# Kernel tuning notes

Measured on AMD Instinct MI355X. Metric: run time of the kernel, lower is better.

Reference implementation:

```python
import jax, jax.numpy as jnp
from jax import lax
import numpy as np

B, C, L, H, W = 2, 64, 16, 64, 64
K = 7
NG = 4  # GroupNorm groups (SpatialGroupNorm(4, channels))


def setup_inputs() -> dict:
    key = jax.random.key(0)
    ks = jax.random.split(key, 16)
    s = lambda i, shape, sc: jax.random.normal(ks[i], shape, jnp.float32) * sc
    return {
        "x": s(0, (B, C, L, H, W), 1.0),
        "dt": jax.random.uniform(ks[1], (B, L), jnp.float32, 0.1, 1.0),
        "W_sp": s(2, (C, C, K, K), 0.02),      # spatial 7x7 conv (OIHW)
        "W_dc": s(3, (C, C), 0.1),             # 1x1x1 depth conv
        "b_dc": jnp.zeros((C,), jnp.float32),
        "gn_g": jnp.ones((C,), jnp.float32),
        "gn_b": jnp.zeros((C,), jnp.float32),
        "W_in": s(4, (2 * C, C), 0.1),         # pw_conv_in 1x1 -> 2C (gated)
        "b_in": jnp.zeros((2 * C,), jnp.float32),
        "W_out": s(5, (C, C), 0.1),            # pw_conv_out 1x1
        "b_out": jnp.zeros((C,), jnp.float32),
        "nu_log": s(6, (C,), 0.5),             # LRU log decay rate
        "theta_log": s(7, (C,), 0.5),          # LRU log frequency
        "c_re": s(8, (C,), 0.5),               # LRU output mix (real)
        "c_im": s(9, (C,), 0.5),               # LRU output mix (imag)
        "d_skip": s(10, (C,), 0.5),            # LRU feedthrough
    }


def reference(x, dt, W_sp, W_dc, b_dc, gn_g, gn_b, W_in, b_in, W_out, b_out,
              nu_log, theta_log, c_re, c_im, d_skip):
    Bb, Cc, Ll, Hh, Ww = x.shape
    pad = W_sp.shape[-1] // 2
    # --- GatedConvBlock: FactorizedPeriodicConv3d (per-frame 2D conv) ---
    xf = x.transpose(0, 2, 1, 3, 4).reshape(Bb * Ll, Cc, Hh, Ww)  # [B*L,C,H,W]
    xp = jnp.pad(xf, ((0, 0), (0, 0), (0, 0), (pad, pad)), mode='wrap')    # circular W
    xp = jnp.pad(xp, ((0, 0), (0, 0), (pad, pad), (0, 0)), mode='edge')    # replicate H
    y = lax.conv_general_dilated(xp, W_sp, (1, 1), 'VALID',
                                 dimension_numbers=('NCHW', 'OIHW', 'NCHW'))
    y = jnp.einsum('nchw,oc->nohw', y, W_dc) + b_dc[None, :, None, None]   # depth 1x1x1
    # --- SpatialGroupNorm (per frame, 4 groups) ---
    g = y.reshape(Bb * Ll, NG, Cc // NG, Hh, Ww)
    mu = g.mean(axis=(2, 3, 4), keepdims=True)
    var = g.var(axis=(2, 3, 4), keepdims=True)
    y = ((g - mu) * lax.rsqrt(var + 1e-5)).reshape(Bb * Ll, Cc, Hh, Ww)
    y = y * gn_g[None, :, None, None] + gn_b[None, :, None, None]
    # --- gated pointwise convs + residual ---
    h = jnp.einsum('nchw,oc->nohw', y, W_in) + b_in[None, :, None, None]
    x1, x2 = jnp.split(h, 2, axis=1)
    z = x1 * jax.nn.sigmoid(x2)
    z = jnp.einsum('nchw,oc->nohw', z, W_out) + b_out[None, :, None, None]
    u = xf + z                                     # residual, [B*L,C,H,W]
    u = u.reshape(Bb, Ll, Cc, Hh, Ww).transpose(1, 0, 2, 3, 4)  # [L,B,C,H,W]
    # --- LRU: dt-dependent complex diagonal recurrence over L ---
    decay = jnp.exp(-jnp.exp(nu_log)[None, None, :] * dt[:, :, None])   # [B,L,C]
    phase = jnp.exp(theta_log)[None, None, :] * dt[:, :, None]          # [B,L,C]
    lam_re = (decay * jnp.cos(phase)).transpose(1, 0, 2)[..., None, None]  # [L,B,C,1,1]
    lam_im = (decay * jnp.sin(phase)).transpose(1, 0, 2)[..., None, None]
    gamma = jnp.sqrt(jnp.maximum(1.0 - decay ** 2, 1e-6)).transpose(1, 0, 2)[..., None, None]
    cr = c_re[None, :, None, None]
    ci = c_im[None, :, None, None]
    ds = d_skip[None, :, None, None]

    def step(carry, inputs):
        h_re, h_im = carry
        ut, lr, li, gm = inputs
        nr = lr * h_re - li * h_im + gm * ut
        ni = li * h_re + lr * h_im
        yt = cr * nr + ci * ni + ds * ut
        return (nr, ni), yt

    init = (jnp.zeros((Bb, Cc, Hh, Ww), x.dtype), jnp.zeros((Bb, Cc, Hh, Ww), x.dtype))
    _, ys = lax.scan(step, init, (u, lam_re, lam_im, gamma))   # ys: [L,B,C,H,W]
    return ys.transpose(1, 2, 0, 3, 4)                         # [B,C,L,H,W]
```

## Files before the change

### kernel.cpp

```cpp
#include <hip/hip_runtime.h>
#include <hip/hip_bf16.h>

typedef short bf16x8 __attribute__((ext_vector_type(8)));
typedef float f32x16 __attribute__((ext_vector_type(16)));

#define B_ 2
#define C_ 64
#define L_ 16
#define N_ 32
#define HW_ 4096

#define BY_WPH  0u
#define BY_WP1  401408u
#define BY_WP2  434176u
#define BY_OFF1 450560u
#define BY_LR   451072u
#define BY_LI   459264u
#define BY_GM   467456u
#define BY_PART 475648u
#define BY_XHI  524288u
#define BY_U    524288u

__device__ __forceinline__ unsigned short f2bf(float v) {
    unsigned int u = __float_as_uint(v);
    unsigned int r = u + 0x7FFFu + ((u >> 16) & 1u);
    return (unsigned short)(r >> 16);
}
__device__ __forceinline__ float bf2f(unsigned short s) {
    return __uint_as_float(((unsigned int)s) << 16);
}

__global__ void k_pack(const float* __restrict__ W_sp, const float* __restrict__ W_dc,
                       unsigned short* __restrict__ WpH) {
    int idx = blockIdx.x * 256 + threadIdx.x;
    if (idx >= 49 * 512) return;
    int lane = idx & 63;
    int ks   = (idx >> 6) & 3;
    int nf   = (idx >> 8) & 1;
    int tap  = idx >> 9;
    int oc   = nf * 32 + (lane & 31);
    int icb  = ks * 16 + (lane >> 5) * 8;
    unsigned short h8[8];
    #pragma unroll
    for (int e = 0; e < 8; ++e) {
        int ic = icb + e;
        float s = 0.f;
        for (int c = 0; c < 64; ++c)
            s += W_dc[oc * 64 + c] * W_sp[(c * 64 + ic) * 49 + tap];
        h8[e] = f2bf(s);
    }
    #pragma unroll
    for (int e = 0; e < 8; ++e) WpH[idx * 8 + e] = h8[e];
}

__global__ void k_prep(const float* __restrict__ W_in, const float* __restrict__ b_in,
                       const float* __restrict__ W_out,
                       const float* __restrict__ gn_g, const float* __restrict__ gn_b,
                       unsigned short* __restrict__ WP1, unsigned short* __restrict__ WP2,
                       float* __restrict__ OFF1) {
    int idx = blockIdx.x * 256 + threadIdx.x;
    if (idx < 2048) {
        int lane = idx & 63, ks = (idx >> 6) & 3, nf = (idx >> 8) & 3, hl = idx >> 10;
        int o = nf * 32 + (lane & 31), cb = ks * 16 + (lane >> 5) * 8;
        #pragma unroll
        for (int e = 0; e < 8; ++e) {
            float v = W_in[o * 64 + cb + e] * gn_g[cb + e];
            unsigned short h = f2bf(v);
            WP1[idx * 8 + e] = hl ? f2bf(v - bf2f(h)) : h;
        }
    } else if (idx < 3072) {
        int i2 = idx - 2048;
        int lane = i2 & 63, ks = (i2 >> 6) & 3, nf = (i2 >> 8) & 1, hl = i2 >> 9;
        int j = nf * 32 + (lane & 31), ob = ks * 16 + (lane >> 5) * 8;
        #pragma unroll
        for (int e = 0; e < 8; ++e) {
            float v = W_out[j * 64 + ob + e];
            unsigned short h = f2bf(v);
            WP2[i2 * 8 + e] = hl ? f2bf(v - bf2f(h)) : h;
        }
    } else if (idx < 3200) {
        int o = idx - 3072;
        float s = b_in[o];
        for (int c = 0; c < 64; ++c) s += W_in[o * 64 + c] * gn_b[c];
        OFF1[o] = s;
    }
}

__global__ void k_lam(const float* __restrict__ dt, const float* __restrict__ nu_log,
                      const float* __restrict__ theta_log,
                      float* __restrict__ lr_t, float* __restrict__ li_t, float* __restrict__ gm_t) {
    int idx = blockIdx.x * 256 + threadIdx.x;
    if (idx >= N_ * C_) return;
    int c = idx & 63, n = idx >> 6;
    float dtv = dt[n];
    float decay = expf(-expf(nu_log[c]) * dtv);
    float phase = expf(theta_log[c]) * dtv;
    lr_t[idx] = decay * cosf(phase);
    li_t[idx] = decay * sinf(phase);
    gm_t[idx] = sqrtf(fmaxf(1.f - decay * decay, 1e-6f));
}

__global__ __launch_bounds__(256) void k_tr(const float* __restrict__ x,
                                            unsigned short* __restrict__ xhi) {
    __shared__ float t[64][129];
    int blk = blockIdx.x;
    int n = blk >> 5, seg = blk & 31;
    int p0 = seg * 128;
    int b = n >> 4, l = n & 15;
    int tid = threadIdx.x;
    for (int i = 0; i < 32; ++i) {
        int idx = i * 256 + tid;
        int ic = idx >> 7, p = idx & 127;
        t[ic][p] = x[(((size_t)(b * 64 + ic) * 16 + l)) * 4096 + p0 + p];
    }
    __syncthreads();
    for (int it = 0; it < 4; ++it) {
        int chunk = it * 256 + tid;
        int p = chunk >> 3, c0 = (chunk & 7) * 8;
        unsigned short h8[8];
        #pragma unroll
        for (int e = 0; e < 8; ++e) h8[e] = f2bf(t[c0 + e][p]);
        size_t off = ((size_t)(n * 4096 + p0 + p)) * 64 + c0;
        *(uint4*)&xhi[off] = *(uint4*)h8;
    }
}

__global__ __launch_bounds__(256, 2) void k_conv(
    const unsigned short* __restrict__ xhi,
    const unsigned short* __restrict__ WpH,
    const float* __restrict__ b_dc, float* __restrict__ y,
    float* __restrict__ part) {
    __shared__ uint4 halo[3904];
    __shared__ float ps[4][8], pq[4][8];
    int tid = threadIdx.x;
    int tile = blockIdx.x;
    int th = tile >> 2, tw = tile & 3;
    int n = blockIdx.y;
    int lane = tid & 63, wid = tid >> 6;
    int dh = (lane >> 4) & 1, dw = lane & 15, kslot = lane >> 5;

    for (int u2 = wid; u2 < 61; u2 += 4) {
        int row = u2 * 8 + (lane >> 3);
        if (row > 483) row = 483;
        int hh = row / 22, ww = row - hh * 22;
        int hs = th * 16 + hh - 3; hs = hs < 0 ? 0 : (hs > 63 ? 63 : hs);
        int wv = (tw * 16 + ww - 3) & 63;
        const uint4* src = (const uint4*)(xhi + ((size_t)n * 4096 + hs * 64 + wv) * 64) + (lane & 7);
        uint4 v = *src;
        *(uint4*)((char*)halo + ((row << 7) + (((lane & 7) ^ (row & 7)) << 4))) = v;
    }
    __syncthreads();

    f32x16 acc[2][2] = {};
    bf16x8 Aa[2][4], Ab[2][4], Ba[2][4], Bb[2][4];

#define LOADA(Areg, khv, kwv) { \
    _Pragma("unroll") for (int m = 0; m < 2; ++m) { \
        int rowb = (wid * 4 + 2 * m + dh + (khv)) * 22 + dw + (kwv); \
        _Pragma("unroll") for (int ks = 0; ks < 4; ++ks) { \
            int byt = (rowb << 7) + (((2 * ks + kslot) ^ (rowb & 7)) << 4); \
            Areg[m][ks] = *(const bf16x8*)((const char*)halo + byt); } } }

#define LOADB(Breg, tap) { \
    const bf16x8* WH = (const bf16x8*)WpH + (size_t)(tap) * 512 + lane; \
    _Pragma("unroll") for (int nf = 0; nf < 2; ++nf) \
        _Pragma("unroll") for (int ks = 0; ks < 4; ++ks) \
            Breg[nf][ks] = WH[(nf * 4 + ks) * 64]; }

#define MFMA_ALL(Areg, Breg) { \
    _Pragma("unroll") for (int ks = 0; ks < 4; ++ks) \
        _Pragma("unroll") for (int m = 0; m < 2; ++m) \
            _Pragma("unroll") for (int nf = 0; nf < 2; ++nf) \
                acc[m][nf] = __builtin_amdgcn_mfma_f32_32x32x16_bf16(Areg[m][ks], Breg[nf][ks], acc[m][nf], 0, 0, 0); }

    int kh = 0, kw = 0;
    LOADA(Aa, 0, 0); LOADB(Ba, 0);
    for (int t = 0; t < 48; t += 2) {
        ++kw; if (kw == 7) { kw = 0; ++kh; }
        LOADA(Ab, kh, kw); LOADB(Bb, t + 1);
        MFMA_ALL(Aa, Ba);
        ++kw; if (kw == 7) { kw = 0; ++kh; }
        LOADA(Aa, kh, kw); LOADB(Ba, t + 2);
        MFMA_ALL(Ab, Bb);
    }
    MFMA_ALL(Aa, Ba);
#undef LOADA
#undef LOADB
#undef MFMA_ALL

    int ocl = lane & 31;
    float sg[2], qg[2];
    #pragma unroll
    for (int nf = 0; nf < 2; ++nf) {
        float bv = b_dc[nf * 32 + ocl];
        float ss = 0.f, qq = 0.f;
        #pragma unroll
        for (int m = 0; m < 2; ++m) {
            #pragma unroll
            for (int j = 0; j < 16; ++j) {
                int r = (j & 3) + 8 * (j >> 2) + 4 * (lane >> 5);
                int h = th * 16 + wid * 4 + 2 * m + (r >> 4);
                int w = tw * 16 + (r & 15);
                float v = acc[m][nf][j] + bv;
                y[((size_t)n * 4096 + h * 64 + w) * 64 + nf * 32 + ocl] = v;
                ss += v; qq += v * v;
            }
        }
        sg[nf] = ss; qg[nf] = qq;
    }
    #pragma unroll
    for (int off = 1; off < 16; off <<= 1) {
        sg[0] += __shfl_xor(sg[0], off);
        qg[0] += __shfl_xor(qg[0], off);
        sg[1] += __shfl_xor(sg[1], off);
        qg[1] += __shfl_xor(qg[1], off);
    }
    if ((lane & 15) == 0) {
        int cl = lane >> 4;
        int g0 = cl & 1, slot = wid * 2 + (cl >> 1);
        ps[g0][slot] = sg[0];     pq[g0][slot] = qg[0];
        ps[2 + g0][slot] = sg[1]; pq[2 + g0][slot] = qg[1];
    }
    __syncthreads();
    if (tid < 4) {
        float ss = 0.f, qq = 0.f;
        #pragma unroll
        for (int k2 = 0; k2 < 8; ++k2) { ss += ps[tid][k2]; qq += pq[tid][k2]; }
        part[((size_t)(n * 16 + tile)) * 8 + tid * 2]     = ss;
        part[((size_t)(n * 16 + tile)) * 8 + tid * 2 + 1] = qq;
    }
}

__global__ __launch_bounds__(256, 1) void k_pw(
    const float* __restrict__ y, const float* __restrict__ part,
    const unsigned short* __restrict__ WP1, const unsigned short* __restrict__ WP2,
    const float* __restrict__ OFF1, const float* __restrict__ b_out,
    const float* __restrict__ x, float* __restrict__ u) {
    __shared__ __align__(16) char lds[4 * 8704];
    int tid = threadIdx.x, lane = tid & 63, wid = tid >> 6;
    int blk = blockIdx.x;
    int n = blk >> 4, pgrp = blk & 15;
    int b = n >> 4, l = n & 15;
    int ocl = lane & 31, hi5 = lane >> 5;
    int pixw = pgrp * 256 + wid * 64;
    char* myl = lds + wid * 8704;

    float mu[4], rsd[4];
    #pragma unroll
    for (int g = 0; g < 4; ++g) {
        float sm = 0.f, sq = 0.f;
        #pragma unroll
        for (int ch = 0; ch < 16; ++ch) {
            sm += part[(n * 16 + ch) * 8 + g * 2];
            sq += part[(n * 16 + ch) * 8 + g * 2 + 1];
        }
        float mean = sm * (1.f / 65536.f);
        float var  = sq * (1.f / 65536.f) - mean * mean;
        mu[g] = mean;
        rsd[g] = rsqrtf(var + 1e-5f);
    }

    const bf16x8* W1 = (const bf16x8*)WP1;
    const bf16x8* W2 = (const bf16x8*)WP2;

    for (int mf = 0; mf < 2; ++mf) {
        int prow = pixw + mf * 32 + ocl;

        bf16x8 A1[4];
        #pragma unroll
        for (int ks = 0; ks < 4; ++ks) {
            const float* yb = &y[(size_t)(n * 4096 + prow) * 64 + ks * 16 + hi5 * 8];
            float4 va = *(const float4*)yb;
            float4 vb = *(const float4*)(yb + 4);
            float m = mu[ks], r = rsd[ks];
            bf16x8 a;
            a[0] = (short)f2bf((va.x - m) * r); a[1] = (short)f2bf((va.y - m) * r);
            a[2] = (short)f2bf((va.z - m) * r); a[3] = (short)f2bf((va.w - m) * r);
            a[4] = (short)f2bf((vb.x - m) * r); a[5] = (short)f2bf((vb.y - m) * r);
            a[6] = (short)f2bf((vb.z - m) * r); a[7] = (short)f2bf((vb.w - m) * r);
            A1[ks] = a;
        }

        f32x16 acc1[4];
        #pragma unroll
        for (int nf = 0; nf < 4; ++nf) {
            float o0 = OFF1[nf * 32 + ocl];
            #pragma unroll
            for (int j = 0; j < 16; ++j) acc1[nf][j] = o0;
        }
        #pragma unroll
        for (int ks = 0; ks < 4; ++ks)
            #pragma unroll
            for (int nf = 0; nf < 4; ++nf) {
                bf16x8 bh = W1[nf * 256 + ks * 64 + lane];
                bf16x8 bl = W1[1024 + nf * 256 + ks * 64 + lane];
                acc1[nf] = __builtin_amdgcn_mfma_f32_32x32x16_bf16(A1[ks], bh, acc1[nf], 0, 0, 0);
                acc1[nf] = __builtin_amdgcn_mfma_f32_32x32x16_bf16(A1[ks], bl, acc1[nf], 0, 0, 0);
            }

        unsigned short* zp = (unsigned short*)myl;
        #pragma unroll
        for (int nf = 0; nf < 2; ++nf)
            #pragma unroll
            for (int j = 0; j < 16; ++j) {
                int r = (j & 3) + 8 * (j >> 2) + 4 * hi5;
                float x1 = acc1[nf][j], x2 = acc1[nf + 2][j];
                float z = x1 / (1.f + __expf(-x2));
                zp[r * 68 + nf * 32 + ocl] = f2bf(z);
            }
        asm volatile("s_waitcnt lgkmcnt(0)" ::: "memory");
        __builtin_amdgcn_sched_barrier(0);

        bf16x8 A2[4];
        #pragma unroll
        for (int ks = 0; ks < 4; ++ks)
            A2[ks] = *(const bf16x8*)(myl + ocl * 136 + ks * 32 + hi5 * 16);

        f32x16 acc2[2];
        #pragma unroll
        for (int nf = 0; nf < 2; ++nf)
            #pragma unroll
            for (int j = 0; j < 16; ++j) acc2[nf][j] = 0.f;
        #pragma unroll
        for (int ks = 0; ks < 4; ++ks)
            #pragma unroll
            for (int nf = 0; nf < 2; ++nf) {
                bf16x8 bh = W2[nf * 256 + ks * 64 + lane];
                bf16x8 bl = W2[512 + nf * 256 + ks * 64 + lane];
                acc2[nf] = __builtin_amdgcn_mfma_f32_32x32x16_bf16(A2[ks], bh, acc2[nf], 0, 0, 0);
                acc2[nf] = __builtin_amdgcn_mfma_f32_32x32x16_bf16(A2[ks], bl, acc2[nf], 0, 0, 0);
            }
        asm volatile("s_waitcnt lgkmcnt(0)" ::: "memory");
        __builtin_amdgcn_sched_barrier(0);

        float* up = (float*)myl;
        #pragma unroll
        for (int nf = 0; nf < 2; ++nf)
            #pragma unroll
            for (int j = 0; j < 16; ++j) {
                int r = (j & 3) + 8 * (j >> 2) + 4 * hi5;
                up[r * 68 + nf * 32 + ocl] = acc2[nf][j];
            }
        asm volatile("s_waitcnt lgkmcnt(0)" ::: "memory");
        __builtin_amdgcn_sched_barrier(0);

        {
            float* rowp = up + ocl * 68 + hi5 * 32;
            float vrow[32];
            #pragma unroll
            for (int c4 = 0; c4 < 8; ++c4) {
                float4 v = *(const float4*)&rowp[c4 * 4];
                vrow[c4 * 4 + 0] = v.x; vrow[c4 * 4 + 1] = v.y;
                vrow[c4 * 4 + 2] = v.z; vrow[c4 * 4 + 3] = v.w;
            }
            int pixg = pixw + mf * 32 + ocl;
            #pragma unroll
            for (int k = 0; k < 32; ++k) {
                int c = hi5 * 32 + k;
                vrow[k] += b_out[c] + x[((size_t)(b * 64 + c) * 16 + l) * 4096 + pixg];
            }
            #pragma unroll
            for (int c4 = 0; c4 < 8; ++c4) {
                float4 v;
                v.x = vrow[c4 * 4 + 0]; v.y = vrow[c4 * 4 + 1];
                v.z = vrow[c4 * 4 + 2]; v.w = vrow[c4 * 4 + 3];
                *(float4*)&rowp[c4 * 4] = v;
            }
        }
        asm volatile("s_waitcnt lgkmcnt(0)" ::: "memory");
        __builtin_amdgcn_sched_barrier(0);

        #pragma unroll
        for (int i = 0; i < 8; ++i) {
            int e = i * 64 + lane;
            int row = e >> 4, c4 = e & 15;
            float4 v = *(const float4*)&up[row * 68 + c4 * 4];
            *(float4*)&u[((size_t)(n * 4096 + pixw + mf * 32 + row)) * 64 + c4 * 4] = v;
        }
        asm volatile("s_waitcnt lgkmcnt(0)" ::: "memory");
        __builtin_amdgcn_sched_barrier(0);
    }
}

__global__ __launch_bounds__(256) void k_scan(
    const float* __restrict__ u, const float* __restrict__ lr_t,
    const float* __restrict__ li_t, const float* __restrict__ gm_t,
    const float* __restrict__ c_re, const float* __restrict__ c_im,
    const float* __restrict__ d_skip, float* __restrict__ out) {
    __shared__ float us[16][68];
    int tid = threadIdx.x;
    int bid = blockIdx.x;
    int b = bid >> 8, h = (bid >> 2) & 63, wq = bid & 3;
    int c4 = tid & 15, p = tid >> 4;
    int w = wq * 16 + p;
    float4 cr4 = *(const float4*)&c_re[c4 * 4];
    float4 ci4 = *(const float4*)&c_im[c4 * 4];
    float4 ds4 = *(const float4*)&d_skip[c4 * 4];
    float hr[4] = {}, hi[4] = {};
    int wp = tid & 15, cc = tid >> 4;
    for (int l = 0; l < 16; ++l) {
        int n = b * 16 + l;
        float4 uv = *(const float4*)&u[((size_t)(n * 4096 + h * 64 + w)) * 64 + c4 * 4];
        float4 lr4 = *(const float4*)&lr_t[n * 64 + c4 * 4];
        float4 li4 = *(const float4*)&li_t[n * 64 + c4 * 4];
        float4 gm4 = *(const float4*)&gm_t[n * 64 + c4 * 4];
        float yv[4];
        {
            float ut = uv.x, lr = lr4.x, li = li4.x;
            float nr = lr * hr[0] - li * hi[0] + gm4.x * ut;
            float ni = li * hr[0] + lr * hi[0];
            yv[0] = cr4.x * nr + ci4.x * ni + ds4.x * ut; hr[0] = nr; hi[0] = ni;
        }
        {
            float ut = uv.y, lr = lr4.y, li = li4.y;
            float nr = lr * hr[1] - li * hi[1] + gm4.y * ut;
            float ni = li * hr[1] + lr * hi[1];
            yv[1] = cr4.y * nr + ci4.y * ni + ds4.y * ut; hr[1] = nr; hi[1] = ni;
        }
        {
            float ut = uv.z, lr = lr4.z, li = li4.z;
            float nr = lr * hr[2] - li * hi[2] + gm4.z * ut;
            float ni = li * hr[2] + lr * hi[2];
            yv[2] = cr4.z * nr + ci4.z * ni + ds4.z * ut; hr[2] = nr; hi[2] = ni;
        }
        {
            float ut = uv.w, lr = lr4.w, li = li4.w;
            float nr = lr * hr[3] - li * hi[3] + gm4.w * ut;
            float ni = li * hr[3] + lr * hi[3];
            yv[3] = cr4.w * nr + ci4.w * ni + ds4.w * ut; hr[3] = nr; hi[3] = ni;
        }
        *(float4*)&us[p][c4 * 4] = *(float4*)yv;
        __syncthreads();
        #pragma unroll
        for (int j = 0; j < 4; ++j) {
            int c = cc * 4 + j;
            out[((size_t)(b * 64 + c) * 16 + l) * 4096 + h * 64 + wq * 16 + wp] = us[wp][c];
        }
        __syncthreads();
    }
}

extern "C" void kernel_launch(void* const* d_in, const int* in_sizes, int n_in,
                              void* d_out, int out_size, void* d_ws, size_t ws_size,
                              hipStream_t stream) {
    const float* x        = (const float*)d_in[0];
    const float* dt       = (const float*)d_in[1];
    const float* W_sp     = (const float*)d_in[2];
    const float* W_dc     = (const float*)d_in[3];
    const float* b_dc     = (const float*)d_in[4];
    const float* gn_g     = (const float*)d_in[5];
    const float* gn_b     = (const float*)d_in[6];
    const float* W_in     = (const float*)d_in[7];
    const float* b_in     = (const float*)d_in[8];
    const float* W_out    = (const float*)d_in[9];
    const float* b_out    = (const float*)d_in[10];
    const float* nu_log   = (const float*)d_in[11];
    const float* theta_log= (const float*)d_in[12];
    const float* c_re     = (const float*)d_in[13];
    const float* c_im     = (const float*)d_in[14];
    const float* d_skip   = (const float*)d_in[15];

    char* ws = (char*)d_ws;
    unsigned short* WpH  = (unsigned short*)(ws + BY_WPH);
    unsigned short* WP1  = (unsigned short*)(ws + BY_WP1);
    unsigned short* WP2  = (unsigned short*)(ws + BY_WP2);
    float* OFF1   = (float*)(ws + BY_OFF1);
    float* lr_t   = (float*)(ws + BY_LR);
    float* li_t   = (float*)(ws + BY_LI);
    float* gm_t   = (float*)(ws + BY_GM);
    float* part   = (float*)(ws + BY_PART);
    unsigned short* xhi = (unsigned short*)(ws + BY_XHI);
    float* u      = (float*)(ws + BY_U);
    float* y      = (float*)d_out;
    float* out    = (float*)d_out;

    hipLaunchKernelGGL(k_pack,    dim3(98),        dim3(256), 0, stream, W_sp, W_dc, WpH);
    hipLaunchKernelGGL(k_prep,    dim3(13),        dim3(256), 0, stream, W_in, b_in, W_out,
                       gn_g, gn_b, WP1, WP2, OFF1);
    hipLaunchKernelGGL(k_lam,     dim3(8),         dim3(256), 0, stream, dt, nu_log, theta_log, lr_t, li_t, gm_t);
    hipLaunchKernelGGL(k_tr,      dim3(1024),      dim3(256), 0, stream, x, xhi);
    hipLaunchKernelGGL(k_conv,    dim3(16, 32),    dim3(256), 0, stream, xhi, WpH, b_dc, y, part);
    hipLaunchKernelGGL(k_pw,      dim3(512),       dim3(256), 0, stream, y, part, WP1, WP2,
                       OFF1, b_out, x, u);
    hipLaunchKernelGGL(k_scan,    dim3(512),       dim3(256), 0, stream, u, lr_t, li_t, gm_t,
                       c_re, c_im, d_skip, out);
}
```

Measured before the change: 143.6 us.

## Split conv tile across eight waves with one M-fragment each

```diff
diff --git a/kernel.cpp b/kernel.cpp
--- a/kernel.cpp
+++ b/kernel.cpp
@@ -125,13 +125,13 @@
     }
 }
 
-__global__ __launch_bounds__(256, 2) void k_conv(
+__global__ __launch_bounds__(512, 4) void k_conv(
     const unsigned short* __restrict__ xhi,
     const unsigned short* __restrict__ WpH,
     const float* __restrict__ b_dc, float* __restrict__ y,
     float* __restrict__ part) {
     __shared__ uint4 halo[3904];
-    __shared__ float ps[4][8], pq[4][8];
+    __shared__ float ps[4][16], pq[4][16];
     int tid = threadIdx.x;
     int tile = blockIdx.x;
     int th = tile >> 2, tw = tile & 3;
@@ -139,7 +139,7 @@
     int lane = tid & 63, wid = tid >> 6;
     int dh = (lane >> 4) & 1, dw = lane & 15, kslot = lane >> 5;
 
-    for (int u2 = wid; u2 < 61; u2 += 4) {
+    for (int u2 = wid; u2 < 61; u2 += 8) {
         int row = u2 * 8 + (lane >> 3);
         if (row > 483) row = 483;
         int hh = row / 22, ww = row - hh * 22;
@@ -151,39 +151,39 @@
     }
     __syncthreads();
 
-    f32x16 acc[2][2] = {};
-    bf16x8 Aa[2][4], Ab[2][4], Ba[2][4], Bb[2][4];
+    f32x16 acc[2] = {};
+    bf16x8 Aa[4], Ab[4], Bc[2][4];
 
 #define LOADA(Areg, khv, kwv) { \
-    _Pragma("unroll") for (int m = 0; m < 2; ++m) { \
-        int rowb = (wid * 4 + 2 * m + dh + (khv)) * 22 + dw + (kwv); \
-        _Pragma("unroll") for (int ks = 0; ks < 4; ++ks) { \
-            int byt = (rowb << 7) + (((2 * ks + kslot) ^ (rowb & 7)) << 4); \
-            Areg[m][ks] = *(const bf16x8*)((const char*)halo + byt); } } }
-
-#define LOADB(Breg, tap) { \
+    int rowb = (wid * 2 + dh + (khv)) * 22 + dw + (kwv); \
+    _Pragma("unroll") for (int ks = 0; ks < 4; ++ks) { \
+        int byt = (rowb << 7) + (((2 * ks + kslot) ^ (rowb & 7)) << 4); \
+        Areg[ks] = *(const bf16x8*)((const char*)halo + byt); } }
+
+#define LOADB(tap) { \
     const bf16x8* WH = (const bf16x8*)WpH + (size_t)(tap) * 512 + lane; \
     _Pragma("unroll") for (int nf = 0; nf < 2; ++nf) \
         _Pragma("unroll") for (int ks = 0; ks < 4; ++ks) \
-            Breg[nf][ks] = WH[(nf * 4 + ks) * 64]; }
-
-#define MFMA_ALL(Areg, Breg) { \
+            Bc[nf][ks] = WH[(nf * 4 + ks) * 64]; }
+
+#define MFMA_ALL(Areg) { \
     _Pragma("unroll") for (int ks = 0; ks < 4; ++ks) \
-        _Pragma("unroll") for (int m = 0; m < 2; ++m) \
-            _Pragma("unroll") for (int nf = 0; nf < 2; ++nf) \
-                acc[m][nf] = __builtin_amdgcn_mfma_f32_32x32x16_bf16(Areg[m][ks], Breg[nf][ks], acc[m][nf], 0, 0, 0); }
+        _Pragma("unroll") for (int nf = 0; nf < 2; ++nf) \
+            acc[nf] = __builtin_amdgcn_mfma_f32_32x32x16_bf16(Areg[ks], Bc[nf][ks], acc[nf], 0, 0, 0); }
 
     int kh = 0, kw = 0;
-    LOADA(Aa, 0, 0); LOADB(Ba, 0);
+    LOADA(Aa, 0, 0); LOADB(0);
     for (int t = 0; t < 48; t += 2) {
         ++kw; if (kw == 7) { kw = 0; ++kh; }
-        LOADA(Ab, kh, kw); LOADB(Bb, t + 1);
-        MFMA_ALL(Aa, Ba);
+        LOADA(Ab, kh, kw);
+        MFMA_ALL(Aa);
+        LOADB(t + 1);
         ++kw; if (kw == 7) { kw = 0; ++kh; }
-        LOADA(Aa, kh, kw); LOADB(Ba, t + 2);
-        MFMA_ALL(Ab, Bb);
-    }
-    MFMA_ALL(Aa, Ba);
+        LOADA(Aa, kh, kw);
+        MFMA_ALL(Ab);
+        LOADB(t + 2);
+    }
+    MFMA_ALL(Aa);
 #undef LOADA
 #undef LOADB
 #undef MFMA_ALL
@@ -195,16 +195,13 @@
         float bv = b_dc[nf * 32 + ocl];
         float ss = 0.f, qq = 0.f;
         #pragma unroll
-        for (int m = 0; m < 2; ++m) {
-            #pragma unroll
-            for (int j = 0; j < 16; ++j) {
-                int r = (j & 3) + 8 * (j >> 2) + 4 * (lane >> 5);
-                int h = th * 16 + wid * 4 + 2 * m + (r >> 4);
-                int w = tw * 16 + (r & 15);
-                float v = acc[m][nf][j] + bv;
-                y[((size_t)n * 4096 + h * 64 + w) * 64 + nf * 32 + ocl] = v;
-                ss += v; qq += v * v;
-            }
+        for (int j = 0; j < 16; ++j) {
+            int r = (j & 3) + 8 * (j >> 2) + 4 * (lane >> 5);
+            int h = th * 16 + wid * 2 + (r >> 4);
+            int w = tw * 16 + (r & 15);
+            float v = acc[nf][j] + bv;
+            y[((size_t)n * 4096 + h * 64 + w) * 64 + nf * 32 + ocl] = v;
+            ss += v; qq += v * v;
         }
         sg[nf] = ss; qg[nf] = qq;
     }
@@ -225,7 +222,7 @@
     if (tid < 4) {
         float ss = 0.f, qq = 0.f;
         #pragma unroll
-        for (int k2 = 0; k2 < 8; ++k2) { ss += ps[tid][k2]; qq += pq[tid][k2]; }
+        for (int k2 = 0; k2 < 16; ++k2) { ss += ps[tid][k2]; qq += pq[tid][k2]; }
         part[((size_t)(n * 16 + tile)) * 8 + tid * 2]     = ss;
         part[((size_t)(n * 16 + tile)) * 8 + tid * 2 + 1] = qq;
     }
@@ -479,7 +476,7 @@
                        gn_g, gn_b, WP1, WP2, OFF1);
     hipLaunchKernelGGL(k_lam,     dim3(8),         dim3(256), 0, stream, dt, nu_log, theta_log, lr_t, li_t, gm_t);
     hipLaunchKernelGGL(k_tr,      dim3(1024),      dim3(256), 0, stream, x, xhi);
-    hipLaunchKernelGGL(k_conv,    dim3(16, 32),    dim3(256), 0, stream, xhi, WpH, b_dc, y, part);
+    hipLaunchKernelGGL(k_conv,    dim3(16, 32),    dim3(512), 0, stream, xhi, WpH, b_dc, y, part);
     hipLaunchKernelGGL(k_pw,      dim3(512),       dim3(256), 0, stream, y, part, WP1, WP2,
                        OFF1, b_out, x, u);
     hipLaunchKernelGGL(k_scan,    dim3(512),       dim3(256), 0, stream, u, lr_t, li_t, gm_t,
```

Result: slower. 152.9 us (+6.4%).
